# Performance work log

Hardware: AMD Instinct MI355X
Metric: run time of the kernel (lower is better)

## Reference

```python
import jax, jax.numpy as jnp
import numpy as np

R = 3                 # search_radius
S2 = (2 * R + 1) ** 2  # 49 correlation channels
VIS_PIXEL_SCALE = 0.1  # arcsec / pixel


def _interp_tokens(tokens, sh, sw, dh, dw):
    # tokens [B, N, D] on (sh, sw) grid -> (dh, dw) grid
    B, N, D = tokens.shape
    x = jnp.transpose(tokens, (0, 2, 1)).reshape(B, D, sh, sw)
    if (sh, sw) != (dh, dw):
        # torch F.interpolate bilinear align_corners=False == jax half-pixel bilinear
        x = jax.image.resize(x, (B, D, dh, dw), method='bilinear')
    return x  # [B, D, dh, dw]


def _l2norm(x, eps=1e-12):
    n = jnp.sqrt(jnp.sum(x * x, axis=1, keepdims=True))
    return x / jnp.maximum(n, eps)


def _corr_volume(q, ref):
    # q, ref: [B, D, H, W]; local cosine-similarity volume [B, S2, H, W]
    q = _l2norm(q)
    ref = _l2norm(ref)
    B, D, H, W = q.shape
    refp = jnp.pad(ref, ((0, 0), (0, 0), (R, R), (R, R)), mode='edge')  # replicate pad
    slices = [
        jnp.sum(q * jax.lax.dynamic_slice(refp, (0, 0, R + dy, R + dx), (B, D, H, W)), axis=1)
        for dy in range(-R, R + 1) for dx in range(-R, R + 1)
    ]
    return jnp.stack(slices, axis=1)


def _conv5(x, w, b):
    y = jax.lax.conv_general_dilated(x, w, (1, 1), 'SAME',
                                     dimension_numbers=('NCHW', 'OIHW', 'NCHW'))
    return y + b[None, :, None, None]


def _refine_net(x, w0, b0, w1, b1, w2, b2):
    h = jax.nn.gelu(_conv5(x, w0, b0), approximate=False)
    h = jax.nn.gelu(_conv5(h, w1, b1), approximate=False)
    return _conv5(h, w2, b2)


def setup_inputs() -> dict:
    key = jax.random.key(0)
    ks = jax.random.split(key, 8)
    B, D = 4, 256
    rubin_tokens = jax.random.normal(ks[0], (B, 64 * 64, D), dtype=jnp.float32)
    vis_tokens = jax.random.normal(ks[1], (B, 128 * 128, D), dtype=jnp.float32)
    in_ch = 2 + S2 + 1  # 52
    hid = 32
    def kaiming(k, shape):
        fan_in = shape[1] * shape[2] * shape[3]
        return jax.random.normal(k, shape, dtype=jnp.float32) / np.sqrt(fan_in)
    w0 = kaiming(ks[2], (hid, in_ch, 5, 5)); b0 = jnp.zeros((hid,), jnp.float32)
    w1 = kaiming(ks[3], (hid, hid, 5, 5));   b1 = jnp.zeros((hid,), jnp.float32)
    w2 = kaiming(ks[4], (2, hid, 5, 5));     b2 = jnp.zeros((2,), jnp.float32)
    log_temp = jnp.asarray(np.log(0.1), dtype=jnp.float32)
    return {
        'rubin_tokens': rubin_tokens, 'vis_tokens': vis_tokens,
        'w0': w0, 'b0': b0, 'w1': w1, 'b1': b1, 'w2': w2, 'b2': b2,
        'log_temp': log_temp,
        'rubin_h': 64, 'rubin_w': 64, 'vis_h': 128, 'vis_w': 128,
        'img_h': 2048, 'img_w': 2048,
    }


def reference(rubin_tokens, vis_tokens, w0, b0, w1, b1, w2, b2, log_temp,
              rubin_h, rubin_w, vis_h, vis_w, img_h, img_w):
    Hc, Wc = max(rubin_h, vis_h), max(rubin_w, vis_w)
    q = _interp_tokens(rubin_tokens, rubin_h, rubin_w, Hc, Wc)  # [B,D,Hc,Wc]
    k = _interp_tokens(vis_tokens, vis_h, vis_w, Hc, Wc)
    corr = _corr_volume(q, k)  # [B,S2,Hc,Wc]

    # soft-argmax over the (2R+1)^2 neighborhood
    coords = jnp.arange(-R, R + 1, dtype=corr.dtype)
    cy, cx = jnp.meshgrid(coords, coords, indexing='ij')
    cy = cy.reshape(1, S2, 1, 1)
    cx = cx.reshape(1, S2, 1, 1)
    temp = jnp.exp(log_temp)
    weights = jax.nn.softmax(corr / temp, axis=1)
    dy = jnp.sum(weights * cy, axis=1, keepdims=True)
    dx = jnp.sum(weights * cx, axis=1, keepdims=True)
    confidence = jnp.max(weights, axis=1, keepdims=True)
    raw_offsets = jnp.concatenate([dy, dx], axis=1)  # [B,2,Hc,Wc]

    x = jnp.concatenate([raw_offsets, corr, confidence], axis=1)  # [B,52,Hc,Wc]
    residual = _refine_net(x, w0, b0, w1, b1, w2, b2)
    refined = raw_offsets + residual

    sky_per_token_y = img_h * VIS_PIXEL_SCALE / Hc
    sky_per_token_x = img_w * VIS_PIXEL_SCALE / Wc
    dra = refined[:, 1:2] * sky_per_token_x
    ddec = refined[:, 0:1] * sky_per_token_y
    # [B,5,Hc,Wc]: dra, ddec, raw_dy, raw_dx, confidence
    return jnp.concatenate([dra, ddec, dy, dx, confidence], axis=1)
```

## Files before the change

kernel.cpp:

```cpp
#include <hip/hip_runtime.h>
#include <math.h>

#define Hh 128
#define Ww 128
#define Dd 256
#define Bb 4
#define HW (Hh*Ww)
#define NPIX (Bb*HW)
#define WP 132

typedef __attribute__((ext_vector_type(8))) short s16x8;
typedef __attribute__((ext_vector_type(4))) float f32x4;

__device__ __forceinline__ unsigned short f2bf(float f) {
    unsigned u = __float_as_uint(f);
    u += 0x7FFF + ((u >> 16) & 1);
    return (unsigned short)(u >> 16);
}

__device__ __forceinline__ float gelu_exact(float v) {
    return 0.5f * v * (1.0f + erff(v * 0.70710678118654752f));
}

#define ZGRAN 1115136
__global__ __launch_bounds__(256) void setup_fill(const float* __restrict__ w0,
                                                  const float* __restrict__ w1,
                                                  const float* __restrict__ w2,
                                                  unsigned short* __restrict__ wb0,
                                                  unsigned short* __restrict__ wb1,
                                                  unsigned short* __restrict__ wb2,
                                                  uint4* __restrict__ zbase) {
    int t = blockIdx.x * 256 + threadIdx.x;
    if (t < ZGRAN) {
        zbase[t] = (uint4){0, 0, 0, 0};
        return;
    }
    int u = t - ZGRAN;
    if (u < 51200) {
        int tap = u >> 11; int r = u & 2047; int n = r >> 6; int k = r & 63;
        wb0[u] = (k < 52) ? f2bf(w0[n * 1300 + k * 25 + tap]) : (unsigned short)0;
    } else if (u < 76800) {
        int v = u - 51200; int tap = v >> 10; int r = v & 1023; int n = r >> 5; int k = r & 31;
        wb1[v] = f2bf(w1[n * 800 + k * 25 + tap]);
    } else if (u < 89600) {
        int v = u - 76800; int tap = v >> 9; int r = v & 511; int n = r >> 5; int k = r & 31;
        wb2[v] = (n < 2) ? f2bf(w2[n * 800 + k * 25 + tap]) : (unsigned short)0;
    }
}

__global__ __launch_bounds__(256) void norm_fused(const float* __restrict__ vis,
                                                  const float* __restrict__ rub,
                                                  unsigned short* __restrict__ kn,
                                                  unsigned short* __restrict__ qn) {
    __shared__ float stok[36 * 260];
    int tid = threadIdx.x;
    int g16 = tid >> 4, l = tid & 15;
    int blk = blockIdx.x;
    if (blk < 4096) {
        int pix = blk * 16 + g16;
        const float* base = vis + (size_t)pix * Dd + l * 4;
        float4 v[4];
#pragma unroll
        for (int i = 0; i < 4; i++) v[i] = *(const float4*)(base + i * 64);
        float ss = 0.f;
#pragma unroll
        for (int i = 0; i < 4; i++)
            ss += v[i].x * v[i].x + v[i].y * v[i].y + v[i].z * v[i].z + v[i].w * v[i].w;
#pragma unroll
        for (int o = 1; o <= 8; o <<= 1) ss += __shfl_xor(ss, o, 64);
        float inv = __builtin_amdgcn_rsqf(fmaxf(ss, 1e-24f));
        unsigned short* op = kn + (size_t)pix * Dd + l * 4;
#pragma unroll
        for (int i = 0; i < 4; i++) {
            ushort4 o4;
            o4.x = f2bf(v[i].x * inv); o4.y = f2bf(v[i].y * inv);
            o4.z = f2bf(v[i].z * inv); o4.w = f2bf(v[i].w * inv);
            *(ushort4*)(op + i * 64) = o4;
        }
    } else {
        int blk2 = blk - 4096;
        int b = blk2 >> 8;
        int rem = blk2 & 255;
        int ty = rem >> 4, tx = rem & 15;
        int oy0 = ty * 8, ox0 = tx * 8;
        int rb = ty * 4 - 1, cb = tx * 4 - 1;
#pragma unroll
        for (int i = 0; i < 9; i++) {
            int g = i * 256 + tid;
            int t = g >> 6, c = g & 63;
            int jy = t / 6, jx = t - jy * 6;
            int gy = min(max(rb + jy, 0), 63);
            int gx = min(max(cb + jx, 0), 63);
            *(float4*)&stok[t * 260 + c * 4] =
                *(const float4*)(rub + ((size_t)(b * 4096 + gy * 64 + gx)) * 256 + c * 4);
        }
        __syncthreads();
        for (int k = 0; k < 4; k++) {
            int pp = g16 * 4 + k;
            int r = pp >> 3, c2 = pp & 7;
            int yo = oy0 + r, xo = ox0 + c2;
            float sy = 0.5f * yo - 0.25f, sx = 0.5f * xo - 0.25f;
            float fyf = floorf(sy), fxf = floorf(sx);
            float fy = sy - fyf, fx = sx - fxf;
            int jy0 = (int)fyf - rb, jx0 = (int)fxf - cb;
            const float* t00 = &stok[(jy0 * 6 + jx0) * 260 + l * 4];
            const float* t01 = t00 + 260;
            const float* t10 = t00 + 6 * 260;
            const float* t11 = t10 + 260;
            float w00 = (1.f - fy) * (1.f - fx), w01 = (1.f - fy) * fx;
            float w10 = fy * (1.f - fx), w11 = fy * fx;
            float4 bv[4];
            float ss = 0.f;
#pragma unroll
            for (int i = 0; i < 4; i++) {
                float4 a = *(const float4*)(t00 + i * 64);
                float4 b1 = *(const float4*)(t01 + i * 64);
                float4 c = *(const float4*)(t10 + i * 64);
                float4 d = *(const float4*)(t11 + i * 64);
                float4 v;
                v.x = w00 * a.x + w01 * b1.x + w10 * c.x + w11 * d.x;
                v.y = w00 * a.y + w01 * b1.y + w10 * c.y + w11 * d.y;
                v.z = w00 * a.z + w01 * b1.z + w10 * c.z + w11 * d.z;
                v.w = w00 * a.w + w01 * b1.w + w10 * c.w + w11 * d.w;
                bv[i] = v;
                ss += v.x * v.x + v.y * v.y + v.z * v.z + v.w * v.w;
            }
#pragma unroll
            for (int o = 1; o <= 8; o <<= 1) ss += __shfl_xor(ss, o, 64);
            float inv = __builtin_amdgcn_rsqf(fmaxf(ss, 1e-24f));
            size_t pix = (size_t)(b << 14) + yo * 128 + xo;
            unsigned short* op = qn + pix * Dd + l * 4;
#pragma unroll
            for (int i = 0; i < 4; i++) {
                ushort4 o4;
                o4.x = f2bf(bv[i].x * inv); o4.y = f2bf(bv[i].y * inv);
                o4.z = f2bf(bv[i].z * inv); o4.w = f2bf(bv[i].w * inv);
                *(ushort4*)(op + i * 64) = o4;
            }
        }
    }
}

__global__ __launch_bounds__(512, 4) void corr_block(const unsigned short* __restrict__ qn,
                                                     const unsigned short* __restrict__ kn,
                                                     const float* __restrict__ log_temp,
                                                     unsigned short* __restrict__ xb,
                                                     float* __restrict__ out) {
    __shared__ char smem[308 * 5 * 16];
    int tid = threadIdx.x;
    int wid = tid >> 6, lane = tid & 63, l15 = lane & 15, quad = lane >> 4;
    int blk = blockIdx.x;
    int b = blk >> 7, rem = blk & 127;
    int y0 = (rem >> 3) << 3, x0 = (rem & 7) << 4;
    int y = y0 + wid;

    const unsigned short* src0; int dst0;
    const unsigned short* src1; int dst1;
    const unsigned short* src2; int dst2; bool hav2;
    {
        int g = tid;
        int px = g >> 2, sub = g & 3;
        int ry = px / 22, rx = px - ry * 22;
        int yy = min(max(y0 - 3 + ry, 0), 127);
        int xx = min(max(x0 - 3 + rx, 0), 127);
        src0 = kn + ((size_t)(b << 14) + yy * 128 + xx) * 256 + sub * 8;
        dst0 = (px * 5 + sub) * 16;
        g = 512 + tid;
        px = g >> 2; sub = g & 3;
        ry = px / 22; rx = px - ry * 22;
        yy = min(max(y0 - 3 + ry, 0), 127);
        xx = min(max(x0 - 3 + rx, 0), 127);
        src1 = kn + ((size_t)(b << 14) + yy * 128 + xx) * 256 + sub * 8;
        dst1 = (px * 5 + sub) * 16;
        g = 1024 + tid;
        hav2 = (g < 1232);
        int gc = hav2 ? g : 1231;
        px = gc >> 2; sub = gc & 3;
        ry = px / 22; rx = px - ry * 22;
        yy = min(max(y0 - 3 + ry, 0), 127);
        xx = min(max(x0 - 3 + rx, 0), 127);
        src2 = kn + ((size_t)(b << 14) + yy * 128 + xx) * 256 + sub * 8;
        dst2 = (px * 5 + sub) * 16;
    }
    int lpixoff[10];
#pragma unroll
    for (int f = 0; f < 10; f++) {
        int p = min(f * 16 + l15, 153);
        int pr = p / 22, pc = p - pr * 22;
        lpixoff[f] = (((wid + pr) * 22 + pc) * 5 + quad) * 16;
    }
    const unsigned short* aptr = qn + ((size_t)(b << 14) + y * 128 + x0 + l15) * 256 + quad * 8;

    f32x4 acc[10];
#pragma unroll
    for (int f = 0; f < 10; f++) acc[f] = (f32x4){0.f, 0.f, 0.f, 0.f};

    uint4 v0 = *(const uint4*)src0;
    uint4 v1 = *(const uint4*)src1;
    uint4 v2 = *(const uint4*)src2;
    s16x8 an = *(const s16x8*)aptr;
    for (int c = 0; c < 8; c++) {
        uint4 w0v = v0, w1v = v1, w2v = v2;
        s16x8 a = an;
        if (c < 7) {
            v0 = *(const uint4*)(src0 + (c + 1) * 32);
            v1 = *(const uint4*)(src1 + (c + 1) * 32);
            v2 = *(const uint4*)(src2 + (c + 1) * 32);
            an = *(const s16x8*)(aptr + (c + 1) * 32);
        }
        __syncthreads();
        *(uint4*)(smem + dst0) = w0v;
        *(uint4*)(smem + dst1) = w1v;
        if (hav2) *(uint4*)(smem + dst2) = w2v;
        __syncthreads();
#pragma unroll
        for (int f = 0; f < 10; f++) {
            s16x8 bf = *(const s16x8*)(smem + lpixoff[f]);
            acc[f] = __builtin_amdgcn_mfma_f32_16x16x32_bf16(a, bf, acc[f], 0, 0, 0);
        }
    }

    float inv_temp = expf(-log_temp[0]);
    float vmax[4] = {-1e30f, -1e30f, -1e30f, -1e30f};
#pragma unroll
    for (int f = 0; f < 10; f++) {
        int n = f * 16 + l15;
        if (n <= 153) {
            int dy = n / 22 - 3;
            int rx = n - (dy + 3) * 22;
#pragma unroll
            for (int i = 0; i < 4; i++) {
                int m = quad * 4 + i;
                int dx = rx - m - 3;
                if ((unsigned)(dx + 3) <= 6u) vmax[i] = fmaxf(vmax[i], acc[f][i]);
            }
        }
    }
#pragma unroll
    for (int o = 1; o <= 8; o <<= 1) {
#pragma unroll
        for (int i = 0; i < 4; i++) vmax[i] = fmaxf(vmax[i], __shfl_xor(vmax[i], o, 64));
    }
    float se[4] = {0, 0, 0, 0}, sey[4] = {0, 0, 0, 0}, sex[4] = {0, 0, 0, 0}, emax[4] = {0, 0, 0, 0};
    unsigned short* xrow = xb + ((size_t)(b * WP + y + 2) * WP + x0 + 2) * 64;
#pragma unroll
    for (int f = 0; f < 10; f++) {
        int n = f * 16 + l15;
        if (n <= 153) {
            int dy = n / 22 - 3;
            int rx = n - (dy + 3) * 22;
#pragma unroll
            for (int i = 0; i < 4; i++) {
                int m = quad * 4 + i;
                int dx = rx - m - 3;
                if ((unsigned)(dx + 3) <= 6u) {
                    float v = acc[f][i];
                    float e = expf((v - vmax[i]) * inv_temp);
                    se[i] += e;
                    sey[i] += e * (float)dy;
                    sex[i] += e * (float)dx;
                    emax[i] = fmaxf(emax[i], e);
                    xrow[(size_t)m * 64 + 2 + (dy + 3) * 7 + (dx + 3)] = f2bf(v);
                }
            }
        }
    }
#pragma unroll
    for (int o = 1; o <= 8; o <<= 1) {
#pragma unroll
        for (int i = 0; i < 4; i++) {
            se[i] += __shfl_xor(se[i], o, 64);
            sey[i] += __shfl_xor(sey[i], o, 64);
            sex[i] += __shfl_xor(sex[i], o, 64);
            emax[i] = fmaxf(emax[i], __shfl_xor(emax[i], o, 64));
        }
    }
    if (l15 == 0) {
#pragma unroll
        for (int i = 0; i < 4; i++) {
            int m = quad * 4 + i;
            float inv_se = 1.0f / se[i];
            float dyv = sey[i] * inv_se, dxv = sex[i] * inv_se, conf = emax[i] * inv_se;
            unsigned short* xp = xrow + (size_t)m * 64;
            xp[0] = f2bf(dyv); xp[1] = f2bf(dxv); xp[51] = f2bf(conf);
            float* op = out + (size_t)b * 5 * HW + y * 128 + x0 + m;
            op[2 * HW] = dyv; op[3 * HW] = dxv; op[4 * HW] = conf;
        }
    }
}

template <int KS, int OC, bool GELU>
__global__ __launch_bounds__(512, 4) void conv_tile(const unsigned short* __restrict__ in,
                                                    const unsigned short* __restrict__ wb,
                                                    const float* __restrict__ bias,
                                                    unsigned short* __restrict__ outp) {
    constexpr int ICP = KS * 32;
    constexpr int NF = OC / 16;
    constexpr int ABYTES = 240 * 5 * 16;
    constexpr int WBYTES = 5 * OC * 5 * 16;
    __shared__ char smem[ABYTES + WBYTES];
    int tid = threadIdx.x;
    int wv = tid >> 6, lane = tid & 63, l15 = lane & 15, quad = lane >> 4;
    int blk = blockIdx.x;
    int b = blk >> 7, rem = blk & 127;
    int ty = rem >> 3, tx = rem & 7;
    int y0 = ty * 8, x0 = tx * 16;

    f32x4 acc[NF];
#pragma unroll
    for (int g = 0; g < NF; g++) acc[g] = (f32x4){0.f, 0.f, 0.f, 0.f};

    for (int ks = 0; ks < KS; ks++) {
        __syncthreads();
#pragma unroll
        for (int i = 0; i < 2; i++) {
            int g = i * 512 + tid;
            if (g < 960) {
                int px = g >> 2, sub = g & 3;
                int r = px / 20, c = px - r * 20;
                *(uint4*)(smem + (px * 5 + sub) * 16) =
                    *(const uint4*)(in + ((size_t)(b * WP + y0 + r) * WP + x0 + c) * ICP + ks * 32 + sub * 8);
            }
        }
        for (int ky = 0; ky < 5; ky++) {
            if (ky > 0) __syncthreads();
            constexpr int WGR = 5 * OC * 4;
#pragma unroll
            for (int i = 0; i < (WGR + 511) / 512; i++) {
                int g = i * 512 + tid;
                if (g < WGR) {
                    int nl = g >> 2, sub = g & 3;
                    *(uint4*)(smem + ABYTES + (nl * 5 + sub) * 16) =
                        *(const uint4*)(wb + ((size_t)(ky * 5 * OC) + nl) * ICP + ks * 32 + sub * 8);
                }
            }
            __syncthreads();
#pragma unroll
            for (int kx = 0; kx < 5; kx++) {
                int abyte = (((wv + ky) * 20 + l15 + kx) * 5 + quad) * 16;
                s16x8 a = *(const s16x8*)(smem + abyte);
#pragma unroll
                for (int g = 0; g < NF; g++) {
                    int wbyte = ABYTES + ((kx * OC + g * 16 + l15) * 5 + quad) * 16;
                    s16x8 bf = *(const s16x8*)(smem + wbyte);
                    acc[g] = __builtin_amdgcn_mfma_f32_16x16x32_bf16(a, bf, acc[g], 0, 0, 0);
                }
            }
        }
    }
    size_t orow = ((size_t)(b * WP + y0 + wv + 2) * WP + x0 + 2) * OC;
#pragma unroll
    for (int g = 0; g < NF; g++) {
        float bv = bias[g * 16 + l15];
#pragma unroll
        for (int r = 0; r < 4; r++) {
            int m = quad * 4 + r;
            float v = acc[g][r] + bv;
            if (GELU) v = gelu_exact(v);
            outp[orow + (size_t)m * OC + g * 16 + l15] = f2bf(v);
        }
    }
}

__global__ __launch_bounds__(512, 4) void conv_final_tile(const unsigned short* __restrict__ in,
                                                          const unsigned short* __restrict__ wb,
                                                          const float* __restrict__ bias,
                                                          float* __restrict__ out) {
    constexpr int ICP = 32, OC = 16;
    constexpr int ABYTES = 240 * 5 * 16;
    constexpr int WBYTES = 5 * OC * 5 * 16;
    __shared__ char smem[ABYTES + WBYTES];
    int tid = threadIdx.x;
    int wv = tid >> 6, lane = tid & 63, l15 = lane & 15, quad = lane >> 4;
    int blk = blockIdx.x;
    int b = blk >> 7, rem = blk & 127;
    int ty = rem >> 3, tx = rem & 7;
    int y0 = ty * 8, x0 = tx * 16;

    f32x4 acc = (f32x4){0.f, 0.f, 0.f, 0.f};
#pragma unroll
    for (int i = 0; i < 2; i++) {
        int g = i * 512 + tid;
        if (g < 960) {
            int px = g >> 2, sub = g & 3;
            int r = px / 20, c = px - r * 20;
            *(uint4*)(smem + (px * 5 + sub) * 16) =
                *(const uint4*)(in + ((size_t)(b * WP + y0 + r) * WP + x0 + c) * ICP + sub * 8);
        }
    }
    for (int ky = 0; ky < 5; ky++) {
        if (ky > 0) __syncthreads();
        constexpr int WGR = 5 * OC * 4;
        {
            int g = tid;
            if (g < WGR) {
                int nl = g >> 2, sub = g & 3;
                *(uint4*)(smem + ABYTES + (nl * 5 + sub) * 16) =
                    *(const uint4*)(wb + ((size_t)(ky * 5 * OC) + nl) * ICP + sub * 8);
            }
        }
        __syncthreads();
#pragma unroll
        for (int kx = 0; kx < 5; kx++) {
            int abyte = (((wv + ky) * 20 + l15 + kx) * 5 + quad) * 16;
            s16x8 a = *(const s16x8*)(smem + abyte);
            int wbyte = ABYTES + ((kx * OC + l15) * 5 + quad) * 16;
            s16x8 bf = *(const s16x8*)(smem + wbyte);
            acc = __builtin_amdgcn_mfma_f32_16x16x32_bf16(a, bf, acc, 0, 0, 0);
        }
    }
    if (l15 < 2) {
        float bv = bias[l15];
#pragma unroll
        for (int r = 0; r < 4; r++) {
            int m = quad * 4 + r;
            size_t p5 = (size_t)b * 5 * HW + (y0 + wv) * Ww + x0 + m;
            float a = acc[r] + bv;
            if (l15 == 0) {
                float dyv = out[p5 + 2 * HW];
                out[p5 + HW] = (dyv + a) * 1.6f;
            } else {
                float dxv = out[p5 + 3 * HW];
                out[p5] = (dxv + a) * 1.6f;
            }
        }
    }
}

extern "C" void kernel_launch(void* const* d_in, const int* in_sizes, int n_in,
                              void* d_out, int out_size, void* d_ws, size_t ws_size,
                              hipStream_t stream) {
    const float* rub = (const float*)d_in[0];
    const float* vis = (const float*)d_in[1];
    const float* w0 = (const float*)d_in[2];
    const float* b0 = (const float*)d_in[3];
    const float* w1 = (const float*)d_in[4];
    const float* b1 = (const float*)d_in[5];
    const float* w2 = (const float*)d_in[6];
    const float* b2 = (const float*)d_in[7];
    const float* log_temp = (const float*)d_in[8];
    float* out = (float*)d_out;

    char* ws = (char*)d_ws;
    size_t off = 0;
    const size_t PADPIX = (size_t)Bb * WP * WP;
    unsigned short* kn = (unsigned short*)(ws + off); off += (size_t)NPIX * Dd * 2;
    unsigned short* qn = (unsigned short*)(ws + off); off += (size_t)NPIX * Dd * 2;
    unsigned short* xbp = (unsigned short*)(ws + off); off += PADPIX * 64 * 2;
    unsigned short* h1p = (unsigned short*)(ws + off); off += PADPIX * 32 * 2;
    unsigned short* h2p = (unsigned short*)(ws + off); off += PADPIX * 32 * 2;
    unsigned short* wb0 = (unsigned short*)(ws + off); off += 51200 * 2;
    unsigned short* wb1 = (unsigned short*)(ws + off); off += 25600 * 2;
    unsigned short* wb2 = (unsigned short*)(ws + off); off += 12800 * 2;

    setup_fill<<<4706, 256, 0, stream>>>(w0, w1, w2, wb0, wb1, wb2, (uint4*)xbp);
    norm_fused<<<5120, 256, 0, stream>>>(vis, rub, kn, qn);
    corr_block<<<512, 512, 0, stream>>>(qn, kn, log_temp, xbp, out);
    conv_tile<2, 32, true><<<512, 512, 0, stream>>>(xbp, wb0, b0, h1p);
    conv_tile<1, 32, true><<<512, 512, 0, stream>>>(h1p, wb1, b1, h2p);
    conv_final_tile<<<512, 512, 0, stream>>>(h2p, wb2, b2, out);
}
```

Baseline: 206.6 us.

## Merge setup and norm kernels, stage corr output in LDS, swizzle conv smem

Measured after the change: 195.7 us. -5.3%, faster.

```diff
diff --git a/kernel.cpp b/kernel.cpp
--- a/kernel.cpp
+++ b/kernel.cpp
@@ -23,41 +23,43 @@
 }
 
 #define ZGRAN 1115136
-__global__ __launch_bounds__(256) void setup_fill(const float* __restrict__ w0,
+__global__ __launch_bounds__(256) void setup_norm(const float* __restrict__ w0,
                                                   const float* __restrict__ w1,
                                                   const float* __restrict__ w2,
                                                   unsigned short* __restrict__ wb0,
                                                   unsigned short* __restrict__ wb1,
                                                   unsigned short* __restrict__ wb2,
-                                                  uint4* __restrict__ zbase) {
-    int t = blockIdx.x * 256 + threadIdx.x;
-    if (t < ZGRAN) {
-        zbase[t] = (uint4){0, 0, 0, 0};
-        return;
-    }
-    int u = t - ZGRAN;
-    if (u < 51200) {
-        int tap = u >> 11; int r = u & 2047; int n = r >> 6; int k = r & 63;
-        wb0[u] = (k < 52) ? f2bf(w0[n * 1300 + k * 25 + tap]) : (unsigned short)0;
-    } else if (u < 76800) {
-        int v = u - 51200; int tap = v >> 10; int r = v & 1023; int n = r >> 5; int k = r & 31;
-        wb1[v] = f2bf(w1[n * 800 + k * 25 + tap]);
-    } else if (u < 89600) {
-        int v = u - 76800; int tap = v >> 9; int r = v & 511; int n = r >> 5; int k = r & 31;
-        wb2[v] = (n < 2) ? f2bf(w2[n * 800 + k * 25 + tap]) : (unsigned short)0;
-    }
-}
-
-__global__ __launch_bounds__(256) void norm_fused(const float* __restrict__ vis,
+                                                  uint4* __restrict__ zbase,
+                                                  const float* __restrict__ vis,
                                                   const float* __restrict__ rub,
                                                   unsigned short* __restrict__ kn,
                                                   unsigned short* __restrict__ qn) {
     __shared__ float stok[36 * 260];
     int tid = threadIdx.x;
+    int blk = blockIdx.x;
+    if (blk < 4706) {
+        int t = blk * 256 + tid;
+        if (t < ZGRAN) {
+            zbase[t] = (uint4){0, 0, 0, 0};
+            return;
+        }
+        int u = t - ZGRAN;
+        if (u < 51200) {
+            int tap = u >> 11; int r = u & 2047; int n = r >> 6; int k = r & 63;
+            wb0[u] = (k < 52) ? f2bf(w0[n * 1300 + k * 25 + tap]) : (unsigned short)0;
+        } else if (u < 76800) {
+            int v = u - 51200; int tap = v >> 10; int r = v & 1023; int n = r >> 5; int k = r & 31;
+            wb1[v] = f2bf(w1[n * 800 + k * 25 + tap]);
+        } else if (u < 89600) {
+            int v = u - 76800; int tap = v >> 9; int r = v & 511; int n = r >> 5; int k = r & 31;
+            wb2[v] = (n < 2) ? f2bf(w2[n * 800 + k * 25 + tap]) : (unsigned short)0;
+        }
+        return;
+    }
+    int nb = blk - 4706;
     int g16 = tid >> 4, l = tid & 15;
-    int blk = blockIdx.x;
-    if (blk < 4096) {
-        int pix = blk * 16 + g16;
+    if (nb < 4096) {
+        int pix = nb * 16 + g16;
         const float* base = vis + (size_t)pix * Dd + l * 4;
         float4 v[4];
 #pragma unroll
@@ -78,7 +80,7 @@
             *(ushort4*)(op + i * 64) = o4;
         }
     } else {
-        int blk2 = blk - 4096;
+        int blk2 = nb - 4096;
         int b = blk2 >> 8;
         int rem = blk2 & 255;
         int ty = rem >> 4, tx = rem & 15;
@@ -146,13 +148,22 @@
                                                      const float* __restrict__ log_temp,
                                                      unsigned short* __restrict__ xb,
                                                      float* __restrict__ out) {
-    __shared__ char smem[308 * 5 * 16];
+    constexpr int ASMEM = 308 * 5 * 16;
+    __shared__ char smem[ASMEM + 128 * 65 * 4];
+    unsigned* sC = (unsigned*)(smem + ASMEM);
     int tid = threadIdx.x;
     int wid = tid >> 6, lane = tid & 63, l15 = lane & 15, quad = lane >> 4;
     int blk = blockIdx.x;
     int b = blk >> 7, rem = blk & 127;
     int y0 = (rem >> 3) << 3, x0 = (rem & 7) << 4;
     int y = y0 + wid;
+
+#pragma unroll
+    for (int i = 0; i < 3; i++) {
+        int g = i * 512 + tid;
+        int px = g / 12, ch = 52 + g - (g / 12) * 12;
+        sC[px * 65 + ch] = 0u;
+    }
 
     const unsigned short* src0; int dst0;
     const unsigned short* src1; int dst1;
@@ -242,7 +253,6 @@
         for (int i = 0; i < 4; i++) vmax[i] = fmaxf(vmax[i], __shfl_xor(vmax[i], o, 64));
     }
     float se[4] = {0, 0, 0, 0}, sey[4] = {0, 0, 0, 0}, sex[4] = {0, 0, 0, 0}, emax[4] = {0, 0, 0, 0};
-    unsigned short* xrow = xb + ((size_t)(b * WP + y + 2) * WP + x0 + 2) * 64;
 #pragma unroll
     for (int f = 0; f < 10; f++) {
         int n = f * 16 + l15;
@@ -260,7 +270,7 @@
                     sey[i] += e * (float)dy;
                     sex[i] += e * (float)dx;
                     emax[i] = fmaxf(emax[i], e);
-                    xrow[(size_t)m * 64 + 2 + (dy + 3) * 7 + (dx + 3)] = f2bf(v);
+                    sC[(wid * 16 + m) * 65 + 2 + (dy + 3) * 7 + (dx + 3)] = (unsigned)f2bf(v);
                 }
             }
         }
@@ -281,11 +291,27 @@
             int m = quad * 4 + i;
             float inv_se = 1.0f / se[i];
             float dyv = sey[i] * inv_se, dxv = sex[i] * inv_se, conf = emax[i] * inv_se;
-            unsigned short* xp = xrow + (size_t)m * 64;
-            xp[0] = f2bf(dyv); xp[1] = f2bf(dxv); xp[51] = f2bf(conf);
+            int px = wid * 16 + m;
+            sC[px * 65 + 0] = (unsigned)f2bf(dyv);
+            sC[px * 65 + 1] = (unsigned)f2bf(dxv);
+            sC[px * 65 + 51] = (unsigned)f2bf(conf);
             float* op = out + (size_t)b * 5 * HW + y * 128 + x0 + m;
             op[2 * HW] = dyv; op[3 * HW] = dxv; op[4 * HW] = conf;
         }
+    }
+    __syncthreads();
+#pragma unroll
+    for (int i = 0; i < 2; i++) {
+        int t2 = i * 512 + tid;
+        int px = t2 >> 3, seg = t2 & 7;
+        const unsigned* sp = sC + px * 65 + seg * 8;
+        uint4 o;
+        o.x = sp[0] | (sp[1] << 16);
+        o.y = sp[2] | (sp[3] << 16);
+        o.z = sp[4] | (sp[5] << 16);
+        o.w = sp[6] | (sp[7] << 16);
+        unsigned short* dst = xb + ((size_t)(b * WP + y0 + (px >> 4) + 2) * WP + x0 + (px & 15) + 2) * 64 + seg * 8;
+        *(uint4*)dst = o;
     }
 }
 
@@ -296,9 +322,10 @@
                                                     unsigned short* __restrict__ outp) {
     constexpr int ICP = KS * 32;
     constexpr int NF = OC / 16;
-    constexpr int ABYTES = 240 * 5 * 16;
-    constexpr int WBYTES = 5 * OC * 5 * 16;
-    __shared__ char smem[ABYTES + WBYTES];
+    constexpr int ABYTES = 240 * 64;
+    constexpr int WROWS = 25 * OC;
+    constexpr int WGRAN = WROWS * 4;
+    __shared__ char smem[ABYTES + WROWS * 64];
     int tid = threadIdx.x;
     int wv = tid >> 6, lane = tid & 63, l15 = lane & 15, quad = lane >> 4;
     int blk = blockIdx.x;
@@ -318,31 +345,30 @@
             if (g < 960) {
                 int px = g >> 2, sub = g & 3;
                 int r = px / 20, c = px - r * 20;
-                *(uint4*)(smem + (px * 5 + sub) * 16) =
+                *(uint4*)(smem + px * 64 + (((sub ^ (px >> 1)) & 3) << 4)) =
                     *(const uint4*)(in + ((size_t)(b * WP + y0 + r) * WP + x0 + c) * ICP + ks * 32 + sub * 8);
             }
         }
+#pragma unroll
+        for (int i = 0; i < (WGRAN + 511) / 512; i++) {
+            int g = i * 512 + tid;
+            if (g < WGRAN) {
+                int nl = g >> 2, sub = g & 3;
+                *(uint4*)(smem + ABYTES + nl * 64 + (((sub ^ (nl >> 1)) & 3) << 4)) =
+                    *(const uint4*)(wb + (size_t)nl * ICP + ks * 32 + sub * 8);
+            }
+        }
+        __syncthreads();
+#pragma unroll
         for (int ky = 0; ky < 5; ky++) {
-            if (ky > 0) __syncthreads();
-            constexpr int WGR = 5 * OC * 4;
-#pragma unroll
-            for (int i = 0; i < (WGR + 511) / 512; i++) {
-                int g = i * 512 + tid;
-                if (g < WGR) {
-                    int nl = g >> 2, sub = g & 3;
-                    *(uint4*)(smem + ABYTES + (nl * 5 + sub) * 16) =
-                        *(const uint4*)(wb + ((size_t)(ky * 5 * OC) + nl) * ICP + ks * 32 + sub * 8);
-                }
-            }
-            __syncthreads();
 #pragma unroll
             for (int kx = 0; kx < 5; kx++) {
-                int abyte = (((wv + ky) * 20 + l15 + kx) * 5 + quad) * 16;
-                s16x8 a = *(const s16x8*)(smem + abyte);
+                int px = (wv + ky) * 20 + l15 + kx;
+                s16x8 a = *(const s16x8*)(smem + px * 64 + (((quad ^ (px >> 1)) & 3) << 4));
 #pragma unroll
                 for (int g = 0; g < NF; g++) {
-                    int wbyte = ABYTES + ((kx * OC + g * 16 + l15) * 5 + quad) * 16;
-                    s16x8 bf = *(const s16x8*)(smem + wbyte);
+                    int row = (ky * 5 + kx) * OC + g * 16 + l15;
+                    s16x8 bf = *(const s16x8*)(smem + ABYTES + row * 64 + (((quad ^ (row >> 1)) & 3) << 4));
                     acc[g] = __builtin_amdgcn_mfma_f32_16x16x32_bf16(a, bf, acc[g], 0, 0, 0);
                 }
             }
@@ -367,9 +393,10 @@
                                                           const float* __restrict__ bias,
                                                           float* __restrict__ out) {
     constexpr int ICP = 32, OC = 16;
-    constexpr int ABYTES = 240 * 5 * 16;
-    constexpr int WBYTES = 5 * OC * 5 * 16;
-    __shared__ char smem[ABYTES + WBYTES];
+    constexpr int ABYTES = 240 * 64;
+    constexpr int WROWS = 25 * OC;
+    constexpr int WGRAN = WROWS * 4;
+    __shared__ char smem[ABYTES + WROWS * 64];
     int tid = threadIdx.x;
     int wv = tid >> 6, lane = tid & 63, l15 = lane & 15, quad = lane >> 4;
     int blk = blockIdx.x;
@@ -377,35 +404,35 @@
     int ty = rem >> 3, tx = rem & 7;
     int y0 = ty * 8, x0 = tx * 16;
 
-    f32x4 acc = (f32x4){0.f, 0.f, 0.f, 0.f};
 #pragma unroll
     for (int i = 0; i < 2; i++) {
         int g = i * 512 + tid;
         if (g < 960) {
             int px = g >> 2, sub = g & 3;
             int r = px / 20, c = px - r * 20;
-            *(uint4*)(smem + (px * 5 + sub) * 16) =
+            *(uint4*)(smem + px * 64 + (((sub ^ (px >> 1)) & 3) << 4)) =
                 *(const uint4*)(in + ((size_t)(b * WP + y0 + r) * WP + x0 + c) * ICP + sub * 8);
         }
     }
+#pragma unroll
+    for (int i = 0; i < 4; i++) {
+        int g = i * 512 + tid;
+        if (g < WGRAN) {
+            int nl = g >> 2, sub = g & 3;
+            *(uint4*)(smem + ABYTES + nl * 64 + (((sub ^ (nl >> 1)) & 3) << 4)) =
+                *(const uint4*)(wb + (size_t)nl * ICP + sub * 8);
+        }
+    }
+    __syncthreads();
+    f32x4 acc = (f32x4){0.f, 0.f, 0.f, 0.f};
+#pragma unroll
     for (int ky = 0; ky < 5; ky++) {
-        if (ky > 0) __syncthreads();
-        constexpr int WGR = 5 * OC * 4;
-        {
-            int g = tid;
-            if (g < WGR) {
-                int nl = g >> 2, sub = g & 3;
-                *(uint4*)(smem + ABYTES + (nl * 5 + sub) * 16) =
-                    *(const uint4*)(wb + ((size_t)(ky * 5 * OC) + nl) * ICP + sub * 8);
-            }
-        }
-        __syncthreads();
 #pragma unroll
         for (int kx = 0; kx < 5; kx++) {
-            int abyte = (((wv + ky) * 20 + l15 + kx) * 5 + quad) * 16;
-            s16x8 a = *(const s16x8*)(smem + abyte);
-            int wbyte = ABYTES + ((kx * OC + l15) * 5 + quad) * 16;
-            s16x8 bf = *(const s16x8*)(smem + wbyte);
+            int px = (wv + ky) * 20 + l15 + kx;
+            s16x8 a = *(const s16x8*)(smem + px * 64 + (((quad ^ (px >> 1)) & 3) << 4));
+            int row = (ky * 5 + kx) * OC + l15;
+            s16x8 bf = *(const s16x8*)(smem + ABYTES + row * 64 + (((quad ^ (row >> 1)) & 3) << 4));
             acc = __builtin_amdgcn_mfma_f32_16x16x32_bf16(a, bf, acc, 0, 0, 0);
         }
     }
@@ -453,8 +480,8 @@
     unsigned short* wb1 = (unsigned short*)(ws + off); off += 25600 * 2;
     unsigned short* wb2 = (unsigned short*)(ws + off); off += 12800 * 2;
 
-    setup_fill<<<4706, 256, 0, stream>>>(w0, w1, w2, wb0, wb1, wb2, (uint4*)xbp);
-    norm_fused<<<5120, 256, 0, stream>>>(vis, rub, kn, qn);
+    setup_norm<<<9826, 256, 0, stream>>>(w0, w1, w2, wb0, wb1, wb2, (uint4*)xbp,
+                                         vis, rub, kn, qn);
     corr_block<<<512, 512, 0, stream>>>(qn, kn, log_temp, xbp, out);
     conv_tile<2, 32, true><<<512, 512, 0, stream>>>(xbp, wb0, b0, h1p);
     conv_tile<1, 32, true><<<512, 512, 0, stream>>>(h1p, wb1, b1, h2p);
```
